# Optimization experiments

Hardware: AMD Instinct MI355X
Metric: run time of the kernel (lower is better)

## Reference

```python
import jax, jax.numpy as jnp
import numpy as np

KH, KW = 3, 3
STRIDE, PAD, DIL = 1, 1, 1
GROUPS, DG = 1, 1
B, C, H, W = 4, 64, 96, 96
O = 64
K = KH * KW


def setup_inputs() -> dict:
    key = jax.random.key(0)
    k1, k2, k3, k4 = jax.random.split(key, 4)
    x = jax.random.normal(k1, (B, C, H, W), dtype=jnp.float32)
    offset = jax.random.normal(k2, (B, DG * 2 * K, H, W), dtype=jnp.float32)
    mask = jax.random.uniform(k3, (B, DG * K, H, W), dtype=jnp.float32)
    stdv = 1.0 / np.sqrt(C * KH * KW)
    weight = jax.random.uniform(k4, (O, C // GROUPS, KH, KW), dtype=jnp.float32,
                                minval=-stdv, maxval=stdv)
    bias = jnp.zeros((O,), dtype=jnp.float32)
    return {"x": x, "offset": offset, "mask": mask, "weight": weight, "bias": bias}


def _dcn(x, offset, mask, weight, bias):
    Bc, Cc, Hc, Wc = x.shape
    Ho = (Hc + 2 * PAD - DIL * (KH - 1) - 1) // STRIDE + 1
    Wo = (Wc + 2 * PAD - DIL * (KW - 1) - 1) // STRIDE + 1
    Cg = Cc // DG
    dt = x.dtype

    # offset channels per deform group: [k, (y,x)] interleaved (mmcv layout)
    off = offset.reshape(Bc, DG, K, 2, Ho, Wo)
    off_y, off_x = off[:, :, :, 0], off[:, :, :, 1]          # [B,DG,K,Ho,Wo]
    m = mask.reshape(Bc, DG, K, Ho, Wo)

    ky = (jnp.arange(K) // KW).astype(dt) * DIL               # kernel tap dy
    kx = (jnp.arange(K) % KW).astype(dt) * DIL                # kernel tap dx
    base_y = (jnp.arange(Ho) * STRIDE - PAD).astype(dt)
    base_x = (jnp.arange(Wo) * STRIDE - PAD).astype(dt)
    py = base_y[None, None, None, :, None] + ky[None, None, :, None, None] + off_y
    px = base_x[None, None, None, None, :] + kx[None, None, :, None, None] + off_x

    y0 = jnp.floor(py)
    x0 = jnp.floor(px)
    ly = py - y0
    lx = px - x0
    y0i = y0.astype(jnp.int32)
    x0i = x0.astype(jnp.int32)

    x_flat = x.reshape(Bc, DG, Cg, Hc * Wc)

    def gather(yi, xi):
        # zero-padding semantics: out-of-range corners contribute 0
        valid = ((yi >= 0) & (yi < Hc) & (xi >= 0) & (xi < Wc)).astype(dt)
        idx = jnp.clip(yi, 0, Hc - 1) * Wc + jnp.clip(xi, 0, Wc - 1)
        idx_b = jnp.broadcast_to(idx.reshape(Bc, DG, 1, K * Ho * Wo),
                                 (Bc, DG, Cg, K * Ho * Wo))
        vals = jnp.take_along_axis(x_flat, idx_b, axis=3)
        return vals.reshape(Bc, DG, Cg, K, Ho, Wo), valid

    v00, m00 = gather(y0i, x0i)
    v01, m01 = gather(y0i, x0i + 1)
    v10, m10 = gather(y0i + 1, x0i)
    v11, m11 = gather(y0i + 1, x0i + 1)

    w00 = ((1 - ly) * (1 - lx) * m00)[:, :, None]             # [B,DG,1,K,Ho,Wo]
    w01 = ((1 - ly) * lx * m01)[:, :, None]
    w10 = (ly * (1 - lx) * m10)[:, :, None]
    w11 = (ly * lx * m11)[:, :, None]

    sampled = v00 * w00 + v01 * w01 + v10 * w10 + v11 * w11   # bilinear
    sampled = sampled * m[:, :, None]                         # mask modulation
    s = sampled.reshape(Bc, Cc, K, Ho, Wo)

    out = jnp.einsum('ock,bckhw->bohw', weight.reshape(O, Cc, K), s)
    return out + bias[None, :, None, None]


def reference(x, offset, mask, weight, bias):
    return _dcn(x, offset, mask, weight, bias)
```

## Files before the change

kernel.cpp:

```cpp
#include <hip/hip_runtime.h>

#define Bn 4
#define Cn 64
#define Hn 96
#define Wn 96
#define On 64
#define Kn 9
#define HWn (Hn*Wn)
#define NT 256
#define TP 16
#define TW (Wn/TP)
#define NBLK (Bn*Hn*TW)
#define SSTRIDE 584
#define NWELEM (18*4*64*8)

typedef __attribute__((ext_vector_type(8))) short bf16x8;
typedef __attribute__((ext_vector_type(4))) float f32x4;

__device__ __forceinline__ unsigned short f2bf(float f) {
    unsigned u = __float_as_uint(f);
    u += 0x7FFFu + ((u >> 16) & 1u);
    return (unsigned short)(u >> 16);
}
__device__ __forceinline__ float bf2f(unsigned short h) {
    return __uint_as_float((unsigned)h << 16);
}

__global__ __launch_bounds__(NT) void prep_kernel(
    const float* __restrict__ x, const float* __restrict__ w,
    unsigned short* __restrict__ xT, unsigned short* __restrict__ wbfA)
{
    __shared__ unsigned short tile[Cn * Wn];
    const int tid = threadIdx.x;
    if (blockIdx.x < Bn * Hn) {
        const int b = blockIdx.x / Hn;
        const int h = blockIdx.x - b * Hn;
        #pragma unroll
        for (int i = 0; i < (Cn * Wn) / NT; ++i) {
            int e = i * NT + tid;
            int c = e / Wn, ww = e - c * Wn;
            tile[c * Wn + ww] = f2bf(x[(((size_t)b * Cn + c) * Hn + h) * Wn + ww]);
        }
        __syncthreads();
        #pragma unroll
        for (int i = 0; i < (Wn * 8) / NT; ++i) {
            int s = i * NT + tid;
            int ww = s >> 3, g = s & 7;
            unsigned short hh[8];
            #pragma unroll
            for (int j = 0; j < 8; ++j) hh[j] = tile[(g * 8 + j) * Wn + ww];
            uint4 pk;
            pk.x = hh[0] | ((unsigned)hh[1] << 16);
            pk.y = hh[2] | ((unsigned)hh[3] << 16);
            pk.z = hh[4] | ((unsigned)hh[5] << 16);
            pk.w = hh[6] | ((unsigned)hh[7] << 16);
            *(uint4*)&xT[(((size_t)b * Hn + h) * Wn + ww) * Cn + g * 8] = pk;
        }
    } else {
        int i = (blockIdx.x - Bn * Hn) * NT + tid;
        if (i < NWELEM) {
            int j  = i & 7;
            int l  = (i >> 3) & 63;
            int wv = (i >> 9) & 3;
            int t  = i >> 11;
            int o  = wv * 16 + (l & 15);
            int kp = t * 32 + (l >> 4) * 8 + j;
            wbfA[i] = f2bf(w[(o * Cn + (kp & 63)) * Kn + (kp >> 6)]);
        }
    }
}

__global__ __launch_bounds__(NT, 6) void dcn4_kernel(
    const unsigned short* __restrict__ xT, const float* __restrict__ offset,
    const float* __restrict__ mask, const float* __restrict__ bias,
    const unsigned short* __restrict__ wbfA, float* __restrict__ out)
{
    __shared__ float4 lwv[Kn * TP];
    __shared__ int4   liv[Kn * TP];
    __shared__ __align__(16) unsigned short Slds[TP * SSTRIDE];

    const int tid = threadIdx.x;
    const int p = blockIdx.x;
    const int v = (p & 7) * (NBLK / 8) + (p >> 3);
    const int b  = v / (Hn * TW);
    int rem      = v - b * (Hn * TW);
    const int ho = rem / TW;
    const int wt = rem - ho * TW;
    const int wo0 = wt * TP;

    if (tid < Kn * TP) {
        int k = tid >> 4;
        int n = tid & 15;
        int wo = wo0 + n;
        float oy = offset[((b * (2*Kn) + 2*k    ) * Hn + ho) * Wn + wo];
        float ox = offset[((b * (2*Kn) + 2*k + 1) * Hn + ho) * Wn + wo];
        float mm = mask  [((b * Kn + k) * Hn + ho) * Wn + wo];
        float py = (float)(ho - 1 + (k / 3)) + oy;
        float px = (float)(wo - 1 + (k % 3)) + ox;
        float y0f = floorf(py), x0f = floorf(px);
        float ly = py - y0f, lx = px - x0f;
        int y0 = (int)y0f, x0i = (int)x0f;
        int y1 = y0 + 1,   x1i = x0i + 1;
        float vy0 = (y0  >= 0 && y0  < Hn) ? 1.f : 0.f;
        float vy1 = (y1  >= 0 && y1  < Hn) ? 1.f : 0.f;
        float vx0 = (x0i >= 0 && x0i < Wn) ? 1.f : 0.f;
        float vx1 = (x1i >= 0 && x1i < Wn) ? 1.f : 0.f;
        int cy0 = min(max(y0, 0),  Hn-1), cy1 = min(max(y1, 0),  Hn-1);
        int cx0 = min(max(x0i, 0), Wn-1), cx1 = min(max(x1i, 0), Wn-1);
        float4 wv;
        wv.x = (1.f - ly) * (1.f - lx) * mm * vy0 * vx0;
        wv.y = (1.f - ly) * lx         * mm * vy0 * vx1;
        wv.z = ly         * (1.f - lx) * mm * vy1 * vx0;
        wv.w = ly         * lx         * mm * vy1 * vx1;
        lwv[tid] = wv;
        liv[tid] = make_int4(cy0 * Wn + cx0, cy0 * Wn + cx1,
                             cy1 * Wn + cx0, cy1 * Wn + cx1);
    }
    __syncthreads();

    {
        const int px = tid >> 4;
        const int g  = tid & 7;
        const int hf = (tid >> 3) & 1;
        const unsigned short* xb = xT + (size_t)b * HWn * Cn + g * 8;
        #pragma unroll
        for (int k = 0; k < Kn; ++k) {
            const int e = k * TP + px;
            float4 wv = lwv[e];
            int4   iv = liv[e];
            int   ia = hf ? iv.z : iv.x;
            int   ib = hf ? iv.w : iv.y;
            float wa = hf ? wv.z : wv.x;
            float wb = hf ? wv.w : wv.y;
            bf16x8 va = *(const bf16x8*)(xb + ((size_t)ia << 6));
            bf16x8 vb = *(const bf16x8*)(xb + ((size_t)ib << 6));
            unsigned short hh[8];
            #pragma unroll
            for (int j = 0; j < 8; ++j) {
                float f = wa * bf2f((unsigned short)va[j]) + wb * bf2f((unsigned short)vb[j]);
                f += __shfl_xor(f, 8);
                hh[j] = f2bf(f);
            }
            if (hf == 0) {
                uint4 pk;
                pk.x = hh[0] | ((unsigned)hh[1] << 16);
                pk.y = hh[2] | ((unsigned)hh[3] << 16);
                pk.z = hh[4] | ((unsigned)hh[5] << 16);
                pk.w = hh[6] | ((unsigned)hh[7] << 16);
                *(uint4*)&Slds[px * SSTRIDE + k * 64 + g * 8] = pk;
            }
        }
    }

    const int wave = tid >> 6;
    const int lane = tid & 63;
    const int n    = lane & 15;
    const int quad = lane >> 4;
    const bf16x8* Af = (const bf16x8*)wbfA;
    bf16x8 aCur = Af[(0 * 4 + wave) * 64 + lane];
    bf16x8 aNxt = Af[(1 * 4 + wave) * 64 + lane];
    __syncthreads();

    f32x4 acc = {0.f, 0.f, 0.f, 0.f};
    #pragma unroll
    for (int t = 0; t < 18; ++t) {
        bf16x8 aUse = aCur;
        aCur = aNxt;
        if (t < 16) aNxt = Af[((t + 2) * 4 + wave) * 64 + lane];
        bf16x8 bfr = *(const bf16x8*)&Slds[n * SSTRIDE + t * 32 + quad * 8];
        acc = __builtin_amdgcn_mfma_f32_16x16x32_bf16(aUse, bfr, acc, 0, 0, 0);
    }

    #pragma unroll
    for (int r = 0; r < 4; ++r) {
        int o = wave * 16 + quad * 4 + r;
        out[(((size_t)b * On + o) * Hn + ho) * Wn + wo0 + n] = acc[r] + bias[o];
    }
}

__global__ __launch_bounds__(NT) void dcn_fallback_kernel(
    const float* __restrict__ x, const float* __restrict__ offset,
    const float* __restrict__ mask, const float* __restrict__ weight,
    const float* __restrict__ bias, float* __restrict__ out)
{
    int idx = blockIdx.x * NT + threadIdx.x;
    if (idx >= Bn * On * HWn) return;
    int wo = idx % Wn;
    int ho = (idx / Wn) % Hn;
    int o  = (idx / HWn) % On;
    int b  = idx / (On * HWn);
    float s = bias[o];
    for (int k = 0; k < Kn; ++k) {
        float oy = offset[((b * (2*Kn) + 2*k    ) * Hn + ho) * Wn + wo];
        float ox = offset[((b * (2*Kn) + 2*k + 1) * Hn + ho) * Wn + wo];
        float mm = mask  [((b * Kn + k) * Hn + ho) * Wn + wo];
        float py = (float)(ho - 1 + (k / 3)) + oy;
        float px = (float)(wo - 1 + (k % 3)) + ox;
        float y0f = floorf(py), x0f = floorf(px);
        float ly = py - y0f, lx = px - x0f;
        int y0 = (int)y0f, x0i = (int)x0f, y1 = y0 + 1, x1i = x0i + 1;
        float vy0 = (y0  >= 0 && y0  < Hn) ? 1.f : 0.f;
        float vy1 = (y1  >= 0 && y1  < Hn) ? 1.f : 0.f;
        float vx0 = (x0i >= 0 && x0i < Wn) ? 1.f : 0.f;
        float vx1 = (x1i >= 0 && x1i < Wn) ? 1.f : 0.f;
        int cy0 = min(max(y0, 0),  Hn-1), cy1 = min(max(y1, 0),  Hn-1);
        int cx0 = min(max(x0i, 0), Wn-1), cx1 = min(max(x1i, 0), Wn-1);
        float w0 = (1.f-ly)*(1.f-lx)*mm*vy0*vx0, w1 = (1.f-ly)*lx*mm*vy0*vx1;
        float w2 = ly*(1.f-lx)*mm*vy1*vx0,       w3 = ly*lx*mm*vy1*vx1;
        int i0 = cy0*Wn+cx0, i1 = cy0*Wn+cx1, i2 = cy1*Wn+cx0, i3 = cy1*Wn+cx1;
        for (int c = 0; c < Cn; ++c) {
            const float* xp = x + ((size_t)b * Cn + c) * HWn;
            float vv = w0*xp[i0] + w1*xp[i1] + w2*xp[i2] + w3*xp[i3];
            s += vv * weight[(o * Cn + c) * Kn + k];
        }
    }
    out[idx] = s;
}

extern "C" void kernel_launch(void* const* d_in, const int* in_sizes, int n_in,
                              void* d_out, int out_size, void* d_ws, size_t ws_size,
                              hipStream_t stream) {
    const float* x      = (const float*)d_in[0];
    const float* offset = (const float*)d_in[1];
    const float* mask   = (const float*)d_in[2];
    const float* weight = (const float*)d_in[3];
    const float* bias   = (const float*)d_in[4];
    float* out = (float*)d_out;

    const size_t xt_bytes = (size_t)Bn * HWn * Cn * sizeof(unsigned short);
    const size_t w_bytes  = (size_t)NWELEM * sizeof(unsigned short);

    if (ws_size >= xt_bytes + w_bytes) {
        unsigned short* xT   = (unsigned short*)d_ws;
        unsigned short* wbfA = (unsigned short*)((char*)d_ws + xt_bytes);
        prep_kernel<<<Bn * Hn + (NWELEM + NT - 1) / NT, NT, 0, stream>>>(x, weight, xT, wbfA);
        dcn4_kernel<<<NBLK, NT, 0, stream>>>(xT, offset, mask, bias, wbfA, out);
    } else {
        dcn_fallback_kernel<<<(Bn * On * HWn + NT - 1) / NT, NT, 0, stream>>>(
            x, offset, mask, weight, bias, out);
    }
}
```

Measured before the change: 91.73 us.

## Split fused deformable conv into separate im2col and MFMA GEMM kernels

Replaces the fused sample-then-GEMM kernel with two kernels. An im2col kernel writes the bilinearly sampled bf16 columns for 48 pixels per block to a global workspace, with each thread now doing all four corners itself instead of pairing with a neighbour through a shuffle. A separate GEMM kernel then reads those columns from global memory for its MFMA tiles. This removes LDS staging and the intra-block sync between sampling and GEMM, but adds about 28 MB of global write and read traffic plus an extra launch, and it needs a larger workspace, otherwise the fallback path runs.

```diff
diff --git a/kernel.cpp b/kernel.cpp
--- a/kernel.cpp
+++ b/kernel.cpp
@@ -8,10 +8,11 @@
 #define Kn 9
 #define HWn (Hn*Wn)
 #define NT 256
-#define TP 16
-#define TW (Wn/TP)
-#define NBLK (Bn*Hn*TW)
-#define SSTRIDE 584
+#define KT 576
+#define TW (Wn/16)
+#define NTILE (Bn*Hn*TW)
+#define IPB 48
+#define NIB (Bn*Hn*2)
 #define NWELEM (18*4*64*8)
 
 typedef __attribute__((ext_vector_type(8))) short bf16x8;
@@ -70,35 +71,32 @@
     }
 }
 
-__global__ __launch_bounds__(NT, 6) void dcn4_kernel(
+__global__ __launch_bounds__(NT) void im2col_kernel(
     const unsigned short* __restrict__ xT, const float* __restrict__ offset,
-    const float* __restrict__ mask, const float* __restrict__ bias,
-    const unsigned short* __restrict__ wbfA, float* __restrict__ out)
-{
-    __shared__ float4 lwv[Kn * TP];
-    __shared__ int4   liv[Kn * TP];
-    __shared__ __align__(16) unsigned short Slds[TP * SSTRIDE];
+    const float* __restrict__ mask, unsigned short* __restrict__ Sg)
+{
+    __shared__ float4 lwv[Kn * IPB];
+    __shared__ int4   liv[Kn * IPB];
 
     const int tid = threadIdx.x;
     const int p = blockIdx.x;
-    const int v = (p & 7) * (NBLK / 8) + (p >> 3);
-    const int b  = v / (Hn * TW);
-    int rem      = v - b * (Hn * TW);
-    const int ho = rem / TW;
-    const int wt = rem - ho * TW;
-    const int wo0 = wt * TP;
-
-    if (tid < Kn * TP) {
-        int k = tid >> 4;
-        int n = tid & 15;
-        int wo = wo0 + n;
+    const int v = (p & 7) * (NIB / 8) + (p >> 3);
+    const int b  = v / (Hn * 2);
+    int r        = v - b * (Hn * 2);
+    const int ho = r >> 1;
+    const int wo0 = (r & 1) * IPB;
+
+    for (int e = tid; e < Kn * IPB; e += NT) {
+        int k  = e / IPB;
+        int px = e - k * IPB;
+        int wo = wo0 + px;
         float oy = offset[((b * (2*Kn) + 2*k    ) * Hn + ho) * Wn + wo];
         float ox = offset[((b * (2*Kn) + 2*k + 1) * Hn + ho) * Wn + wo];
         float mm = mask  [((b * Kn + k) * Hn + ho) * Wn + wo];
         float py = (float)(ho - 1 + (k / 3)) + oy;
-        float px = (float)(wo - 1 + (k % 3)) + ox;
-        float y0f = floorf(py), x0f = floorf(px);
-        float ly = py - y0f, lx = px - x0f;
+        float px_ = (float)(wo - 1 + (k % 3)) + ox;
+        float y0f = floorf(py), x0f = floorf(px_);
+        float ly = py - y0f, lx = px_ - x0f;
         int y0 = (int)y0f, x0i = (int)x0f;
         int y1 = y0 + 1,   x1i = x0i + 1;
         float vy0 = (y0  >= 0 && y0  < Hn) ? 1.f : 0.f;
@@ -112,63 +110,73 @@
         wv.y = (1.f - ly) * lx         * mm * vy0 * vx1;
         wv.z = ly         * (1.f - lx) * mm * vy1 * vx0;
         wv.w = ly         * lx         * mm * vy1 * vx1;
-        lwv[tid] = wv;
-        liv[tid] = make_int4(cy0 * Wn + cx0, cy0 * Wn + cx1,
-                             cy1 * Wn + cx0, cy1 * Wn + cx1);
+        lwv[e] = wv;
+        liv[e] = make_int4(cy0 * Wn + cx0, cy0 * Wn + cx1,
+                           cy1 * Wn + cx0, cy1 * Wn + cx1);
     }
     __syncthreads();
 
-    {
-        const int px = tid >> 4;
-        const int g  = tid & 7;
-        const int hf = (tid >> 3) & 1;
-        const unsigned short* xb = xT + (size_t)b * HWn * Cn + g * 8;
-        #pragma unroll
-        for (int k = 0; k < Kn; ++k) {
-            const int e = k * TP + px;
+    const unsigned short* xb = xT + (size_t)b * HWn * Cn;
+    unsigned short* sb = Sg + ((size_t)b * HWn + (size_t)ho * Wn + wo0) * KT;
+
+    #pragma unroll
+    for (int it = 0; it < 14; ++it) {
+        int tau = it * NT + tid;
+        if (tau < Kn * IPB * 8) {
+            int g  = tau & 7;
+            int e  = tau >> 3;
+            int px = e % IPB;
             float4 wv = lwv[e];
             int4   iv = liv[e];
-            int   ia = hf ? iv.z : iv.x;
-            int   ib = hf ? iv.w : iv.y;
-            float wa = hf ? wv.z : wv.x;
-            float wb = hf ? wv.w : wv.y;
-            bf16x8 va = *(const bf16x8*)(xb + ((size_t)ia << 6));
-            bf16x8 vb = *(const bf16x8*)(xb + ((size_t)ib << 6));
+            bf16x8 v0 = *(const bf16x8*)(xb + ((size_t)iv.x << 6) + g * 8);
+            bf16x8 v1 = *(const bf16x8*)(xb + ((size_t)iv.y << 6) + g * 8);
+            bf16x8 v2 = *(const bf16x8*)(xb + ((size_t)iv.z << 6) + g * 8);
+            bf16x8 v3 = *(const bf16x8*)(xb + ((size_t)iv.w << 6) + g * 8);
             unsigned short hh[8];
             #pragma unroll
             for (int j = 0; j < 8; ++j) {
-                float f = wa * bf2f((unsigned short)va[j]) + wb * bf2f((unsigned short)vb[j]);
-                f += __shfl_xor(f, 8);
+                float f = wv.x * bf2f((unsigned short)v0[j]) + wv.y * bf2f((unsigned short)v1[j])
+                        + wv.z * bf2f((unsigned short)v2[j]) + wv.w * bf2f((unsigned short)v3[j]);
                 hh[j] = f2bf(f);
             }
-            if (hf == 0) {
-                uint4 pk;
-                pk.x = hh[0] | ((unsigned)hh[1] << 16);
-                pk.y = hh[2] | ((unsigned)hh[3] << 16);
-                pk.z = hh[4] | ((unsigned)hh[5] << 16);
-                pk.w = hh[6] | ((unsigned)hh[7] << 16);
-                *(uint4*)&Slds[px * SSTRIDE + k * 64 + g * 8] = pk;
-            }
-        }
-    }
-
+            uint4 pk;
+            pk.x = hh[0] | ((unsigned)hh[1] << 16);
+            pk.y = hh[2] | ((unsigned)hh[3] << 16);
+            pk.z = hh[4] | ((unsigned)hh[5] << 16);
+            pk.w = hh[6] | ((unsigned)hh[7] << 16);
+            int k = e / IPB;
+            *(uint4*)&sb[(size_t)px * KT + k * 64 + g * 8] = pk;
+        }
+    }
+}
+
+__global__ __launch_bounds__(NT) void gemm_kernel(
+    const unsigned short* __restrict__ Sg, const unsigned short* __restrict__ wbfA,
+    const float* __restrict__ bias, float* __restrict__ out)
+{
+    const int tid  = threadIdx.x;
     const int wave = tid >> 6;
     const int lane = tid & 63;
     const int n    = lane & 15;
     const int quad = lane >> 4;
+
+    const int p = blockIdx.x;
+    const int v = (p & 7) * (NTILE / 8) + (p >> 3);
+    const int b  = v / (Hn * TW);
+    int rem      = v - b * (Hn * TW);
+    const int ho = rem / TW;
+    const int wt = rem - ho * TW;
+    const int wo0 = wt * 16;
+
+    const unsigned short* Srow = Sg + ((size_t)b * HWn + (size_t)ho * Wn + wo0 + n) * KT;
     const bf16x8* Af = (const bf16x8*)wbfA;
-    bf16x8 aCur = Af[(0 * 4 + wave) * 64 + lane];
-    bf16x8 aNxt = Af[(1 * 4 + wave) * 64 + lane];
-    __syncthreads();
 
     f32x4 acc = {0.f, 0.f, 0.f, 0.f};
     #pragma unroll
     for (int t = 0; t < 18; ++t) {
-        bf16x8 aUse = aCur;
-        aCur = aNxt;
-        if (t < 16) aNxt = Af[((t + 2) * 4 + wave) * 64 + lane];
-        bf16x8 bfr = *(const bf16x8*)&Slds[n * SSTRIDE + t * 32 + quad * 8];
-        acc = __builtin_amdgcn_mfma_f32_16x16x32_bf16(aUse, bfr, acc, 0, 0, 0);
+        bf16x8 a  = Af[(t * 4 + wave) * 64 + lane];
+        bf16x8 bf = *(const bf16x8*)(Srow + t * 32 + quad * 8);
+        acc = __builtin_amdgcn_mfma_f32_16x16x32_bf16(a, bf, acc, 0, 0, 0);
     }
 
     #pragma unroll
@@ -229,12 +237,15 @@
 
     const size_t xt_bytes = (size_t)Bn * HWn * Cn * sizeof(unsigned short);
     const size_t w_bytes  = (size_t)NWELEM * sizeof(unsigned short);
-
-    if (ws_size >= xt_bytes + w_bytes) {
+    const size_t sg_bytes = (size_t)Bn * HWn * KT * sizeof(unsigned short);
+
+    if (ws_size >= xt_bytes + w_bytes + sg_bytes) {
         unsigned short* xT   = (unsigned short*)d_ws;
         unsigned short* wbfA = (unsigned short*)((char*)d_ws + xt_bytes);
+        unsigned short* Sg   = (unsigned short*)((char*)d_ws + xt_bytes + w_bytes);
         prep_kernel<<<Bn * Hn + (NWELEM + NT - 1) / NT, NT, 0, stream>>>(x, weight, xT, wbfA);
-        dcn4_kernel<<<NBLK, NT, 0, stream>>>(xT, offset, mask, bias, wbfA, out);
+        im2col_kernel<<<NIB, NT, 0, stream>>>(xT, offset, mask, Sg);
+        gemm_kernel<<<NTILE, NT, 0, stream>>>(Sg, wbfA, bias, out);
     } else {
         dcn_fallback_kernel<<<(Bn * On * HWn + NT - 1) / NT, NT, 0, stream>>>(
             x, offset, mask, weight, bias, out);
```

Result: slower. 115.3 us (+25.7%).

## Restructure DCN gather per-wave with 4-corner loads and removed shuffle

Applied to the files above, without the earlier changes.

Each wave now computes bilinear coefficients for its own 4 output pixels, so one block-wide barrier before the gather is removed. Each lane handles 4 channels and loads all four corners directly, dropping the cross-lane shuffle reduction and the half-idle store. Weight-fragment prefetch is hoisted to the kernel start with a 3-deep register ring, and the occupancy hint drops from 6 to 4 blocks. The trade is more, smaller (8-byte) global gathers per lane and higher register use.

```diff
diff --git a/kernel.cpp b/kernel.cpp
--- a/kernel.cpp
+++ b/kernel.cpp
@@ -15,6 +15,7 @@
 #define NWELEM (18*4*64*8)
 
 typedef __attribute__((ext_vector_type(8))) short bf16x8;
+typedef __attribute__((ext_vector_type(4))) short bf16x4;
 typedef __attribute__((ext_vector_type(4))) float f32x4;
 
 __device__ __forceinline__ unsigned short f2bf(float f) {
@@ -24,6 +25,9 @@
 }
 __device__ __forceinline__ float bf2f(unsigned short h) {
     return __uint_as_float((unsigned)h << 16);
+}
+__device__ __forceinline__ unsigned cvtpk(float a, float b) {
+    return (unsigned)f2bf(a) | ((unsigned)f2bf(b) << 16);
 }
 
 __global__ __launch_bounds__(NT) void prep_kernel(
@@ -70,16 +74,19 @@
     }
 }
 
-__global__ __launch_bounds__(NT, 6) void dcn4_kernel(
+__global__ __launch_bounds__(NT, 4) void dcn5_kernel(
     const unsigned short* __restrict__ xT, const float* __restrict__ offset,
     const float* __restrict__ mask, const float* __restrict__ bias,
     const unsigned short* __restrict__ wbfA, float* __restrict__ out)
 {
-    __shared__ float4 lwv[Kn * TP];
-    __shared__ int4   liv[Kn * TP];
+    __shared__ float4 lwv[4][36];
+    __shared__ int4   liv[4][36];
     __shared__ __align__(16) unsigned short Slds[TP * SSTRIDE];
 
-    const int tid = threadIdx.x;
+    const int tid  = threadIdx.x;
+    const int wave = tid >> 6;
+    const int lane = tid & 63;
+
     const int p = blockIdx.x;
     const int v = (p & 7) * (NBLK / 8) + (p >> 3);
     const int b  = v / (Hn * TW);
@@ -88,10 +95,16 @@
     const int wt = rem - ho * TW;
     const int wo0 = wt * TP;
 
-    if (tid < Kn * TP) {
-        int k = tid >> 4;
-        int n = tid & 15;
-        int wo = wo0 + n;
+    const bf16x8* Af = (const bf16x8*)wbfA;
+    bf16x8 aReg[3];
+    aReg[0] = Af[(0 * 4 + wave) * 64 + lane];
+    aReg[1] = Af[(1 * 4 + wave) * 64 + lane];
+    aReg[2] = Af[(2 * 4 + wave) * 64 + lane];
+
+    if (lane < 36) {
+        int k  = lane >> 2;
+        int pl = lane & 3;
+        int wo = wo0 + wave * 4 + pl;
         float oy = offset[((b * (2*Kn) + 2*k    ) * Hn + ho) * Wn + wo];
         float ox = offset[((b * (2*Kn) + 2*k + 1) * Hn + ho) * Wn + wo];
         float mm = mask  [((b * Kn + k) * Hn + ho) * Wn + wo];
@@ -112,63 +125,47 @@
         wv.y = (1.f - ly) * lx         * mm * vy0 * vx1;
         wv.z = ly         * (1.f - lx) * mm * vy1 * vx0;
         wv.w = ly         * lx         * mm * vy1 * vx1;
-        lwv[tid] = wv;
-        liv[tid] = make_int4(cy0 * Wn + cx0, cy0 * Wn + cx1,
-                             cy1 * Wn + cx0, cy1 * Wn + cx1);
-    }
-    __syncthreads();
+        lwv[wave][lane] = wv;
+        liv[wave][lane] = make_int4(cy0 * Wn + cx0, cy0 * Wn + cx1,
+                                    cy1 * Wn + cx0, cy1 * Wn + cx1);
+    }
 
     {
-        const int px = tid >> 4;
-        const int g  = tid & 7;
-        const int hf = (tid >> 3) & 1;
-        const unsigned short* xb = xT + (size_t)b * HWn * Cn + g * 8;
+        const int pl  = lane >> 4;
+        const int q   = lane & 15;
+        const int gpx = wave * 4 + pl;
+        const unsigned short* xb = xT + (size_t)b * HWn * Cn + q * 4;
         #pragma unroll
         for (int k = 0; k < Kn; ++k) {
-            const int e = k * TP + px;
-            float4 wv = lwv[e];
-            int4   iv = liv[e];
-            int   ia = hf ? iv.z : iv.x;
-            int   ib = hf ? iv.w : iv.y;
-            float wa = hf ? wv.z : wv.x;
-            float wb = hf ? wv.w : wv.y;
-            bf16x8 va = *(const bf16x8*)(xb + ((size_t)ia << 6));
-            bf16x8 vb = *(const bf16x8*)(xb + ((size_t)ib << 6));
-            unsigned short hh[8];
+            float4 wv = lwv[wave][k * 4 + pl];
+            int4   iv = liv[wave][k * 4 + pl];
+            bf16x4 v0 = *(const bf16x4*)(xb + ((size_t)iv.x << 6));
+            bf16x4 v1 = *(const bf16x4*)(xb + ((size_t)iv.y << 6));
+            bf16x4 v2 = *(const bf16x4*)(xb + ((size_t)iv.z << 6));
+            bf16x4 v3 = *(const bf16x4*)(xb + ((size_t)iv.w << 6));
+            float f[4];
             #pragma unroll
-            for (int j = 0; j < 8; ++j) {
-                float f = wa * bf2f((unsigned short)va[j]) + wb * bf2f((unsigned short)vb[j]);
-                f += __shfl_xor(f, 8);
-                hh[j] = f2bf(f);
+            for (int j = 0; j < 4; ++j) {
+                f[j] = wv.x * bf2f((unsigned short)v0[j]) + wv.y * bf2f((unsigned short)v1[j])
+                     + wv.z * bf2f((unsigned short)v2[j]) + wv.w * bf2f((unsigned short)v3[j]);
             }
-            if (hf == 0) {
-                uint4 pk;
-                pk.x = hh[0] | ((unsigned)hh[1] << 16);
-                pk.y = hh[2] | ((unsigned)hh[3] << 16);
-                pk.z = hh[4] | ((unsigned)hh[5] << 16);
-                pk.w = hh[6] | ((unsigned)hh[7] << 16);
-                *(uint4*)&Slds[px * SSTRIDE + k * 64 + g * 8] = pk;
-            }
-        }
-    }
-
-    const int wave = tid >> 6;
-    const int lane = tid & 63;
+            uint2 pk;
+            pk.x = cvtpk(f[0], f[1]);
+            pk.y = cvtpk(f[2], f[3]);
+            *(uint2*)&Slds[gpx * SSTRIDE + k * 64 + q * 4] = pk;
+        }
+    }
+    __syncthreads();
+
     const int n    = lane & 15;
     const int quad = lane >> 4;
-    const bf16x8* Af = (const bf16x8*)wbfA;
-    bf16x8 aCur = Af[(0 * 4 + wave) * 64 + lane];
-    bf16x8 aNxt = Af[(1 * 4 + wave) * 64 + lane];
-    __syncthreads();
-
     f32x4 acc = {0.f, 0.f, 0.f, 0.f};
     #pragma unroll
     for (int t = 0; t < 18; ++t) {
-        bf16x8 aUse = aCur;
-        aCur = aNxt;
-        if (t < 16) aNxt = Af[((t + 2) * 4 + wave) * 64 + lane];
-        bf16x8 bfr = *(const bf16x8*)&Slds[n * SSTRIDE + t * 32 + quad * 8];
-        acc = __builtin_amdgcn_mfma_f32_16x16x32_bf16(aUse, bfr, acc, 0, 0, 0);
+        bf16x8 aUse = aReg[t % 3];
+        if (t + 3 < 18) aReg[t % 3] = Af[((t + 3) * 4 + wave) * 64 + lane];
+        bf16x8 bf = *(const bf16x8*)&Slds[n * SSTRIDE + t * 32 + quad * 8];
+        acc = __builtin_amdgcn_mfma_f32_16x16x32_bf16(aUse, bf, acc, 0, 0, 0);
     }
 
     #pragma unroll
@@ -234,7 +231,7 @@
         unsigned short* xT   = (unsigned short*)d_ws;
         unsigned short* wbfA = (unsigned short*)((char*)d_ws + xt_bytes);
         prep_kernel<<<Bn * Hn + (NWELEM + NT - 1) / NT, NT, 0, stream>>>(x, weight, xT, wbfA);
-        dcn4_kernel<<<NBLK, NT, 0, stream>>>(xT, offset, mask, bias, wbfA, out);
+        dcn5_kernel<<<NBLK, NT, 0, stream>>>(xT, offset, mask, bias, wbfA, out);
     } else {
         dcn_fallback_kernel<<<(Bn * On * HWn + NT - 1) / NT, NT, 0, stream>>>(
             x, offset, mask, weight, bias, out);
```

New measurement: 91.33 us. No clear change (-0.4%).
